# Kernel tuning notes

Measured on AMD Instinct MI355X. Metric: run time of the kernel, lower is better.

Reference implementation:

```python
import jax, jax.numpy as jnp
import numpy as np

NUM_HEADS = 16
EPS = 1e-6


def _phi(x):
    # Positive feature map: ELU + 1
    return jax.nn.elu(x) + 1.0


def setup_inputs() -> dict:
    key = jax.random.key(0)
    ks = jax.random.split(key, 5)
    B, L, D = 4, 8192, 1024
    scale = 0.02
    return {
        "x": jax.random.normal(ks[0], (B, L, D), dtype=jnp.float32),
        "Wq": jax.random.normal(ks[1], (D, D), dtype=jnp.float32) * scale,
        "Wk": jax.random.normal(ks[2], (D, D), dtype=jnp.float32) * scale,
        "Wv": jax.random.normal(ks[3], (D, D), dtype=jnp.float32) * scale,
        "Wo": jax.random.normal(ks[4], (D, D), dtype=jnp.float32) * scale,
    }


def reference(x, Wq, Wk, Wv, Wo):
    B, L, D = x.shape
    H = NUM_HEADS
    dh = D // H
    # Projections (bias-free linear layers)
    Q = x @ Wq
    K = x @ Wk
    V = x @ Wv
    # Split heads: (B, H, L, dh)
    Qh = Q.reshape(B, L, H, dh).transpose(0, 2, 1, 3)
    Kh = K.reshape(B, L, H, dh).transpose(0, 2, 1, 3)
    Vh = V.reshape(B, L, H, dh).transpose(0, 2, 1, 3)
    Qf = _phi(Qh)
    Kf = _phi(Kh)
    # Global key-value reduction over time: (B, H, dh, dh)
    Kv = jnp.einsum('bhlm,bhln->bhmn', Kf, Vh)
    # Key normalizer: (B, H, dh)
    K1 = jnp.sum(Kf, axis=2)
    # Numerator / denominator
    num = jnp.einsum('bhlm,bhmn->bhln', Qf, Kv)
    den = jnp.einsum('bhlm,bhm->bhl', Qf, K1) + EPS
    out = num / den[..., None]
    out = out.transpose(0, 2, 1, 3).reshape(B, L, D)
    return out @ Wo
```

## Files before the change

### kernel.cpp

```cpp
#include <hip/hip_runtime.h>
#include <stdint.h>
#include <stddef.h>

typedef __bf16 bf16;
typedef __attribute__((ext_vector_type(8))) __bf16 bf16x8;
typedef __attribute__((ext_vector_type(4))) __bf16 bf16x4;
typedef __attribute__((ext_vector_type(4))) float f32x4;

#define ATT_EPS 1e-6f

__device__ __forceinline__ void lds16(const void* g, void* l) {
    __builtin_amdgcn_global_load_lds(
        (const __attribute__((address_space(1))) void*)g,
        (__attribute__((address_space(3))) void*)l, 16, 0, 0);
}

__device__ __forceinline__ void swizzle_uv(int lin, int& u, int& v) {
    u = (lin & 7) | ((lin >> 6) << 3);
    v = (lin >> 3) & 7;
}

__global__ __launch_bounds__(256) void cvt_bf16(const float4* __restrict__ in,
                                                bf16x4* __restrict__ out, int n4) {
    int i = blockIdx.x * 256 + threadIdx.x;
    if (i < n4) {
        float4 v = in[i];
        bf16x4 o;
        o.x = (bf16)v.x; o.y = (bf16)v.y; o.z = (bf16)v.z; o.w = (bf16)v.w;
        out[i] = o;
    }
}

__global__ __launch_bounds__(256) void transpose_w(const float* __restrict__ W,
                                                   bf16* __restrict__ Wt) {
    __shared__ float tile[32][33];
    const int bx = blockIdx.x * 32, by = blockIdx.y * 32;
    const int tx = threadIdx.x, ty = threadIdx.y;
#pragma unroll
    for (int j = 0; j < 32; j += 8)
        tile[ty + j][tx] = W[(size_t)(by + ty + j) * 1024 + bx + tx];
    __syncthreads();
#pragma unroll
    for (int j = 0; j < 32; j += 8)
        Wt[(size_t)(bx + ty + j) * 1024 + by + tx] = (bf16)tile[tx][ty + j];
}

template <int MODE>
__global__ __launch_bounds__(256) void gemm_bt(const bf16* __restrict__ A, int lda,
                                               const bf16* __restrict__ B, int ldb,
                                               void* __restrict__ C, int ldc, int K) {
    constexpr int EP_STRIDE = 136;
    constexpr int SMEM_ELEMS = (MODE == 2) ? 128 * EP_STRIDE : 8192;
    __shared__ bf16 smem[SMEM_ELEMS] __attribute__((aligned(16)));
    bf16* sA = smem;
    bf16* sB = smem + 4096;
    const int t = threadIdx.x;
    const int wave = t >> 6;
    const int lane = t & 63;
    int u, v;
    swizzle_uv(blockIdx.x, u, v);
    const int tileM = u * 128;
    const int tileN = v * 128;
    const int wm = (wave >> 1) * 64;
    const int wn = (wave & 1) * 64;

    f32x4 acc[4][4] = {};

    const int srow = t >> 2;
    const int scol = (t & 3) * 8;
    const bf16* a0 = A + (size_t)(tileM + srow) * lda + scol;
    const bf16* a1 = A + (size_t)(tileM + 64 + srow) * lda + scol;
    const bf16* b0 = B + (size_t)(tileN + srow) * ldb + scol;
    const bf16* b1 = B + (size_t)(tileN + 64 + srow) * ldb + scol;
    bf16* dA0 = sA + wave * 512;
    bf16* dA1 = sA + 2048 + wave * 512;
    bf16* dB0 = sB + wave * 512;
    bf16* dB1 = sB + 2048 + wave * 512;

    const int rm = lane & 15;
    const int qk = (lane >> 4) * 8;

    for (int k0 = 0; k0 < K; k0 += 32) {
        lds16(a0 + k0, dA0);
        lds16(a1 + k0, dA1);
        lds16(b0 + k0, dB0);
        lds16(b1 + k0, dB1);
        __builtin_amdgcn_s_waitcnt(0);
        __syncthreads();
        bf16x8 af[4], bfr[4];
#pragma unroll
        for (int mi = 0; mi < 4; mi++)
            af[mi] = *(const bf16x8*)&sA[(wm + mi * 16 + rm) * 32 + qk];
#pragma unroll
        for (int ni = 0; ni < 4; ni++)
            bfr[ni] = *(const bf16x8*)&sB[(wn + ni * 16 + rm) * 32 + qk];
#pragma unroll
        for (int mi = 0; mi < 4; mi++)
#pragma unroll
            for (int ni = 0; ni < 4; ni++)
                acc[mi][ni] = __builtin_amdgcn_mfma_f32_16x16x32_bf16(
                    af[mi], bfr[ni], acc[mi][ni], 0, 0, 0);
        __syncthreads();
    }

    const int row0 = (lane >> 4) * 4;
    const int col = lane & 15;
    if (MODE == 0) {
#pragma unroll
        for (int mi = 0; mi < 4; mi++)
#pragma unroll
            for (int ni = 0; ni < 4; ni++)
#pragma unroll
                for (int r = 0; r < 4; r++) {
                    int gm = tileM + wm + mi * 16 + row0 + r;
                    int gn = tileN + wn + ni * 16 + col;
                    ((float*)C)[(size_t)gm * ldc + gn] = acc[mi][ni][r];
                }
    } else {
#pragma unroll
        for (int mi = 0; mi < 4; mi++)
#pragma unroll
            for (int ni = 0; ni < 4; ni++)
#pragma unroll
                for (int r = 0; r < 4; r++) {
                    float val = acc[mi][ni][r];
                    val = (val > 0.f) ? (val + 1.f) : __expf(val);
                    smem[(wm + mi * 16 + row0 + r) * EP_STRIDE + wn + ni * 16 + col] =
                        (bf16)val;
                }
        __syncthreads();
        const int er = t >> 4, ec = (t & 15) * 8;
#pragma unroll
        for (int i = 0; i < 8; i++) {
            int row = er + i * 16;
            *(bf16x8*)&((bf16*)C)[(size_t)(tileM + row) * ldc + tileN + ec] =
                *(const bf16x8*)&smem[row * EP_STRIDE + ec];
        }
    }
}

__global__ __launch_bounds__(256, 2) void kv_proj(const bf16* __restrict__ Wkt,
                                                  const bf16* __restrict__ Wvt,
                                                  const bf16* __restrict__ xb,
                                                  bf16* __restrict__ Kft,
                                                  bf16* __restrict__ Vt) {
    constexpr int EP_STRIDE = 136;
    __shared__ bf16 smem[128 * EP_STRIDE] __attribute__((aligned(16)));
    bf16* sK = smem;
    bf16* sV = smem + 4096;
    bf16* sX = smem + 8192;
    const int t = threadIdx.x;
    const int wave = t >> 6;
    const int lane = t & 63;
    int u, v;
    swizzle_uv(blockIdx.x, u, v);
    const int tileM = v * 128;
    const int tileN = u * 128;
    const int wm = (wave >> 1) * 64;
    const int wn = (wave & 1) * 64;

    f32x4 accK[4][4] = {};
    f32x4 accV[4][4] = {};

    const int srow = t >> 2;
    const int scol = (t & 3) * 8;
    const bf16* k0p = Wkt + (size_t)(tileM + srow) * 1024 + scol;
    const bf16* k1p = k0p + (size_t)64 * 1024;
    const bf16* v0p = Wvt + (size_t)(tileM + srow) * 1024 + scol;
    const bf16* v1p = v0p + (size_t)64 * 1024;
    const bf16* x0p = xb + (size_t)(tileN + srow) * 1024 + scol;
    const bf16* x1p = x0p + (size_t)64 * 1024;
    bf16* dK0 = sK + wave * 512;
    bf16* dK1 = sK + 2048 + wave * 512;
    bf16* dV0 = sV + wave * 512;
    bf16* dV1 = sV + 2048 + wave * 512;
    bf16* dX0 = sX + wave * 512;
    bf16* dX1 = sX + 2048 + wave * 512;

    const int rm = lane & 15;
    const int qk = (lane >> 4) * 8;

    for (int k0 = 0; k0 < 1024; k0 += 32) {
        lds16(k0p + k0, dK0);
        lds16(k1p + k0, dK1);
        lds16(v0p + k0, dV0);
        lds16(v1p + k0, dV1);
        lds16(x0p + k0, dX0);
        lds16(x1p + k0, dX1);
        __builtin_amdgcn_s_waitcnt(0);
        __syncthreads();
        bf16x8 bfr[4], afK[4], afV[4];
#pragma unroll
        for (int ni = 0; ni < 4; ni++)
            bfr[ni] = *(const bf16x8*)&sX[(wn + ni * 16 + rm) * 32 + qk];
#pragma unroll
        for (int mi = 0; mi < 4; mi++) {
            afK[mi] = *(const bf16x8*)&sK[(wm + mi * 16 + rm) * 32 + qk];
            afV[mi] = *(const bf16x8*)&sV[(wm + mi * 16 + rm) * 32 + qk];
        }
#pragma unroll
        for (int mi = 0; mi < 4; mi++)
#pragma unroll
            for (int ni = 0; ni < 4; ni++) {
                accK[mi][ni] = __builtin_amdgcn_mfma_f32_16x16x32_bf16(
                    afK[mi], bfr[ni], accK[mi][ni], 0, 0, 0);
                accV[mi][ni] = __builtin_amdgcn_mfma_f32_16x16x32_bf16(
                    afV[mi], bfr[ni], accV[mi][ni], 0, 0, 0);
            }
        __syncthreads();
    }

    const int row0 = (lane >> 4) * 4;
    const int col = lane & 15;
    const int er = t >> 4, ec = (t & 15) * 8;

#pragma unroll
    for (int mi = 0; mi < 4; mi++)
#pragma unroll
        for (int ni = 0; ni < 4; ni++)
#pragma unroll
            for (int r = 0; r < 4; r++) {
                float val = accK[mi][ni][r];
                val = (val > 0.f) ? (val + 1.f) : __expf(val);
                smem[(wm + mi * 16 + row0 + r) * EP_STRIDE + wn + ni * 16 + col] =
                    (bf16)val;
            }
    __syncthreads();
#pragma unroll
    for (int i = 0; i < 8; i++) {
        int row = er + i * 16;
        *(bf16x8*)&Kft[(size_t)(tileM + row) * 32768 + tileN + ec] =
            *(const bf16x8*)&smem[row * EP_STRIDE + ec];
    }
    __syncthreads();
#pragma unroll
    for (int mi = 0; mi < 4; mi++)
#pragma unroll
        for (int ni = 0; ni < 4; ni++)
#pragma unroll
            for (int r = 0; r < 4; r++)
                smem[(wm + mi * 16 + row0 + r) * EP_STRIDE + wn + ni * 16 + col] =
                    (bf16)accV[mi][ni][r];
    __syncthreads();
#pragma unroll
    for (int i = 0; i < 8; i++) {
        int row = er + i * 16;
        *(bf16x8*)&Vt[(size_t)(tileM + row) * 32768 + tileN + ec] =
            *(const bf16x8*)&smem[row * EP_STRIDE + ec];
    }
}

__global__ __launch_bounds__(256) void kv_reduce(const bf16* __restrict__ Kft,
                                                 const bf16* __restrict__ Vt,
                                                 float* __restrict__ Kv) {
    const int chunk = blockIdx.x;
    const int bh = blockIdx.y;
    const int b = bh >> 4, h = bh & 15;
    __shared__ bf16 sA[64 * 32] __attribute__((aligned(16)));
    __shared__ bf16 sB[64 * 32] __attribute__((aligned(16)));
    const int t = threadIdx.x, wave = t >> 6, lane = t & 63;
    const size_t cbase = (size_t)b * 8192 + (size_t)chunk * 1024;
    const int srow = t >> 2, scol = (t & 3) * 8;
    const bf16* a0 = Kft + (size_t)(h * 64 + srow) * 32768 + cbase + scol;
    const bf16* b0 = Vt + (size_t)(h * 64 + srow) * 32768 + cbase + scol;
    bf16* dA = sA + wave * 512;
    bf16* dB = sB + wave * 512;
    const int rm = lane & 15, qk = (lane >> 4) * 8;

    f32x4 acc[4] = {};
    f32x4 acc1 = {0.f, 0.f, 0.f, 0.f};
    bf16x8 ones;
#pragma unroll
    for (int j = 0; j < 8; j++) ones[j] = (bf16)1.0f;

    for (int k0 = 0; k0 < 1024; k0 += 32) {
        lds16(a0 + k0, dA);
        lds16(b0 + k0, dB);
        __builtin_amdgcn_s_waitcnt(0);
        __syncthreads();
        bf16x8 af = *(const bf16x8*)&sA[(wave * 16 + rm) * 32 + qk];
        bf16x8 bfr[4];
#pragma unroll
        for (int ni = 0; ni < 4; ni++)
            bfr[ni] = *(const bf16x8*)&sB[(ni * 16 + rm) * 32 + qk];
#pragma unroll
        for (int ni = 0; ni < 4; ni++)
            acc[ni] = __builtin_amdgcn_mfma_f32_16x16x32_bf16(af, bfr[ni], acc[ni], 0, 0, 0);
        acc1 = __builtin_amdgcn_mfma_f32_16x16x32_bf16(af, ones, acc1, 0, 0, 0);
        __syncthreads();
    }

    float* out = Kv + bh * 65 * 64;
    const int row0 = (lane >> 4) * 4, col = lane & 15;
    const int m0 = wave * 16 + row0;
#pragma unroll
    for (int ni = 0; ni < 4; ni++)
#pragma unroll
        for (int r = 0; r < 4; r++)
            atomicAdd(&out[(ni * 16 + col) * 64 + m0 + r], acc[ni][r]);
    if (col == 0) {
#pragma unroll
        for (int r = 0; r < 4; r++) atomicAdd(&out[64 * 64 + m0 + r], acc1[r]);
    }
}

__global__ __launch_bounds__(256) void attn_out(const bf16* __restrict__ Qf,
                                                const float* __restrict__ Kv,
                                                bf16* __restrict__ attn) {
    const int lt = blockIdx.x;
    const int bh = blockIdx.y;
    const int b = bh >> 4, h = bh & 15;
    constexpr int EP_STRIDE = 80;
    __shared__ bf16 smem[13312] __attribute__((aligned(16)));
    __shared__ float den[128];
    bf16* sQ = smem;
    bf16* sB = smem + 8192;
    const int t = threadIdx.x, wave = t >> 6, lane = t & 63;
    const int qrow = t >> 3, qc = (t & 7) * 8;
    const bf16* qp = Qf + (size_t)(b * 8192 + lt * 128 + qrow) * 1024 + h * 64 + qc;
#pragma unroll
    for (int i = 0; i < 4; i++)
        lds16(qp + (size_t)i * 32 * 1024, sQ + i * 2048 + wave * 512);
    const float* kv = Kv + bh * 65 * 64;
    for (int idx = t; idx < 80 * 64; idx += 256) {
        int n = idx >> 6, k2 = idx & 63;
        sB[idx] = (n < 65) ? (bf16)kv[n * 64 + k2] : (bf16)0.f;
    }
    __builtin_amdgcn_s_waitcnt(0);
    __syncthreads();

    f32x4 acc[2][5] = {};
    const int rm = lane & 15, qk = (lane >> 4) * 8;
#pragma unroll
    for (int k0 = 0; k0 < 64; k0 += 32) {
        bf16x8 af[2], bfr[5];
#pragma unroll
        for (int mi = 0; mi < 2; mi++)
            af[mi] = *(const bf16x8*)&sQ[(wave * 32 + mi * 16 + rm) * 64 + k0 + qk];
#pragma unroll
        for (int ni = 0; ni < 5; ni++)
            bfr[ni] = *(const bf16x8*)&sB[(ni * 16 + rm) * 64 + k0 + qk];
#pragma unroll
        for (int mi = 0; mi < 2; mi++)
#pragma unroll
            for (int ni = 0; ni < 5; ni++)
                acc[mi][ni] = __builtin_amdgcn_mfma_f32_16x16x32_bf16(
                    af[mi], bfr[ni], acc[mi][ni], 0, 0, 0);
    }

    const int row0 = (lane >> 4) * 4, col = lane & 15;
    if (col == 0) {
#pragma unroll
        for (int mi = 0; mi < 2; mi++)
#pragma unroll
            for (int r = 0; r < 4; r++)
                den[wave * 32 + mi * 16 + row0 + r] = acc[mi][4][r] + ATT_EPS;
    }
    __syncthreads();
#pragma unroll
    for (int mi = 0; mi < 2; mi++)
#pragma unroll
        for (int ni = 0; ni < 4; ni++)
#pragma unroll
            for (int r = 0; r < 4; r++) {
                int rl = wave * 32 + mi * 16 + row0 + r;
                smem[rl * EP_STRIDE + ni * 16 + col] =
                    (bf16)(acc[mi][ni][r] / den[rl]);
            }
    __syncthreads();
    const int er = t >> 3, ec = (t & 7) * 8;
#pragma unroll
    for (int i = 0; i < 4; i++) {
        int row = er + i * 32;
        *(bf16x8*)&attn[(size_t)(b * 8192 + lt * 128 + row) * 1024 + h * 64 + ec] =
            *(const bf16x8*)&smem[row * EP_STRIDE + ec];
    }
}

extern "C" void kernel_launch(void* const* d_in, const int* in_sizes, int n_in,
                              void* d_out, int out_size, void* d_ws, size_t ws_size,
                              hipStream_t stream) {
    const float* x  = (const float*)d_in[0];
    const float* Wq = (const float*)d_in[1];
    const float* Wk = (const float*)d_in[2];
    const float* Wv = (const float*)d_in[3];
    const float* Wo = (const float*)d_in[4];

    char* ws = (char*)d_ws;
    bf16* xb  = (bf16*)ws;
    bf16* Qf  = (bf16*)(ws + ((size_t)64 << 20));
    bf16* Kft = (bf16*)(ws + ((size_t)128 << 20));
    bf16* Vt  = (bf16*)(ws + ((size_t)192 << 20));
    bf16* Wqt = (bf16*)(ws + ((size_t)256 << 20));
    bf16* Wkt = Wqt + 1024 * 1024;
    bf16* Wvt = Wkt + 1024 * 1024;
    bf16* Wot = Wvt + 1024 * 1024;
    float* Kv = (float*)(Wot + 1024 * 1024);
    bf16* attn = xb;

    cvt_bf16<<<8388608 / 256, 256, 0, stream>>>((const float4*)x, (bf16x4*)xb, 8388608);
    dim3 tb(32, 8);
    transpose_w<<<dim3(32, 32), tb, 0, stream>>>(Wq, Wqt);
    transpose_w<<<dim3(32, 32), tb, 0, stream>>>(Wk, Wkt);
    transpose_w<<<dim3(32, 32), tb, 0, stream>>>(Wv, Wvt);
    transpose_w<<<dim3(32, 32), tb, 0, stream>>>(Wo, Wot);
    hipMemsetAsync(Kv, 0, (size_t)64 * 65 * 64 * sizeof(float), stream);

    gemm_bt<2><<<2048, 256, 0, stream>>>(xb, 1024, Wqt, 1024, Qf, 1024, 1024);
    kv_proj<<<2048, 256, 0, stream>>>(Wkt, Wvt, xb, Kft, Vt);
    kv_reduce<<<dim3(8, 64), 256, 0, stream>>>(Kft, Vt, Kv);
    attn_out<<<dim3(64, 64), 256, 0, stream>>>(Qf, Kv, attn);
    gemm_bt<0><<<2048, 256, 0, stream>>>(attn, 1024, Wot, 1024, d_out, 1024, 1024);
}
```

Baseline: 689.7 us.

## Replace GEMMs with 256x256 tiled, 4-stage pipelined, swizzled-LDS kernel

Replaces the 128x128 single-buffered GEMM and the fused K/V projection kernel with one 256x256-tile, 512-thread GEMM. It uses a 4-deep LDS ring buffer with async global-to-LDS loads, XOR-swizzled LDS layout, MFMA priority bumps and an XCD-aware block remap. The K and V projections become two separate launches, so x is read twice instead of once. The 128KB LDS footprint limits occupancy to one block per CU, and correctness depends on the swizzle and vmcnt counting being right.

```diff
diff --git a/kernel.cpp b/kernel.cpp
--- a/kernel.cpp
+++ b/kernel.cpp
@@ -13,11 +13,6 @@
     __builtin_amdgcn_global_load_lds(
         (const __attribute__((address_space(1))) void*)g,
         (__attribute__((address_space(3))) void*)l, 16, 0, 0);
-}
-
-__device__ __forceinline__ void swizzle_uv(int lin, int& u, int& v) {
-    u = (lin & 7) | ((lin >> 6) << 3);
-    v = (lin >> 3) & 7;
 }
 
 __global__ __launch_bounds__(256) void cvt_bf16(const float4* __restrict__ in,
@@ -46,207 +41,119 @@
 }
 
 template <int MODE>
-__global__ __launch_bounds__(256) void gemm_bt(const bf16* __restrict__ A, int lda,
+__global__ __launch_bounds__(512) void gemm256(const bf16* __restrict__ A, int lda,
                                                const bf16* __restrict__ B, int ldb,
-                                               void* __restrict__ C, int ldc, int K) {
-    constexpr int EP_STRIDE = 136;
-    constexpr int SMEM_ELEMS = (MODE == 2) ? 128 * EP_STRIDE : 8192;
-    __shared__ bf16 smem[SMEM_ELEMS] __attribute__((aligned(16)));
-    bf16* sA = smem;
-    bf16* sB = smem + 4096;
+                                               void* __restrict__ C, int ldc,
+                                               int K, int fast_m, int fl2) {
+    __shared__ bf16 smem[65536] __attribute__((aligned(16)));
     const int t = threadIdx.x;
-    const int wave = t >> 6;
-    const int lane = t & 63;
-    int u, v;
-    swizzle_uv(blockIdx.x, u, v);
-    const int tileM = u * 128;
-    const int tileN = v * 128;
-    const int wm = (wave >> 1) * 64;
-    const int wn = (wave & 1) * 64;
-
-    f32x4 acc[4][4] = {};
-
-    const int srow = t >> 2;
-    const int scol = (t & 3) * 8;
-    const bf16* a0 = A + (size_t)(tileM + srow) * lda + scol;
-    const bf16* a1 = A + (size_t)(tileM + 64 + srow) * lda + scol;
-    const bf16* b0 = B + (size_t)(tileN + srow) * ldb + scol;
-    const bf16* b1 = B + (size_t)(tileN + 64 + srow) * ldb + scol;
-    bf16* dA0 = sA + wave * 512;
-    bf16* dA1 = sA + 2048 + wave * 512;
-    bf16* dB0 = sB + wave * 512;
-    bf16* dB1 = sB + 2048 + wave * 512;
-
-    const int rm = lane & 15;
-    const int qk = (lane >> 4) * 8;
-
-    for (int k0 = 0; k0 < K; k0 += 32) {
-        lds16(a0 + k0, dA0);
-        lds16(a1 + k0, dA1);
-        lds16(b0 + k0, dB0);
-        lds16(b1 + k0, dB1);
-        __builtin_amdgcn_s_waitcnt(0);
-        __syncthreads();
-        bf16x8 af[4], bfr[4];
-#pragma unroll
-        for (int mi = 0; mi < 4; mi++)
-            af[mi] = *(const bf16x8*)&sA[(wm + mi * 16 + rm) * 32 + qk];
-#pragma unroll
-        for (int ni = 0; ni < 4; ni++)
-            bfr[ni] = *(const bf16x8*)&sB[(wn + ni * 16 + rm) * 32 + qk];
-#pragma unroll
-        for (int mi = 0; mi < 4; mi++)
+    const int wave = t >> 6, lane = t & 63;
+    const int q8 = gridDim.x >> 3;
+    const int wg = (blockIdx.x & 7) * q8 + (blockIdx.x >> 3);
+    const int f = wg & ((1 << fl2) - 1), s = wg >> fl2;
+    const int mt = fast_m ? f : s, nt = fast_m ? s : f;
+    const int tileM = mt << 8, tileN = nt << 8;
+    const int wm = wave >> 2, wn = wave & 3;
+
+    int rowS[2], colS[2];
+#pragma unroll
+    for (int j = 0; j < 2; j++) {
+        int off = t * 16 + j * 8192;
+        int o = off & 1023;
+        int op = o ^ (((o >> 9) & 1) << 5);
+        rowS[j] = (off >> 10) * 16 + (op >> 6);
+        colS[j] = (op & 63) >> 1;
+    }
+    const int rm = lane & 15, qq = lane >> 4;
+    const int foff = ((rm * 64 + qq * 16) ^ ((rm >> 3) << 5)) >> 1;
+
+    f32x4 acc[8][4] = {};
+
+#define STAGE(tt)                                                              \
+    {                                                                          \
+        bf16* sA_ = smem + ((tt) & 3) * 16384;                                 \
+        bf16* sB_ = sA_ + 8192;                                                \
+        const int k0_ = (tt) << 5;                                             \
+        _Pragma("unroll") for (int j = 0; j < 2; j++) {                        \
+            lds16(A + (size_t)(tileM + rowS[j]) * lda + k0_ + colS[j],         \
+                  sA_ + wave * 512 + j * 4096);                                \
+            lds16(B + (size_t)(tileN + rowS[j]) * ldb + k0_ + colS[j],         \
+                  sB_ + wave * 512 + j * 4096);                                \
+        }                                                                      \
+    }
+
+#define COMPUTE(tt)                                                            \
+    {                                                                          \
+        const bf16* pA_ = smem + ((tt) & 3) * 16384 + wm * 4096 + foff;        \
+        const bf16* pB_ = smem + ((tt) & 3) * 16384 + 8192 + wn * 2048 + foff; \
+        bf16x8 af_[8], bv_[4];                                                 \
+        _Pragma("unroll") for (int mi = 0; mi < 8; mi++)                       \
+            af_[mi] = *(const bf16x8*)(pA_ + mi * 512);                        \
+        _Pragma("unroll") for (int ni = 0; ni < 4; ni++)                       \
+            bv_[ni] = *(const bf16x8*)(pB_ + ni * 512);                        \
+        __builtin_amdgcn_s_setprio(1);                                         \
+        _Pragma("unroll") for (int mi = 0; mi < 8; mi++)                       \
+            _Pragma("unroll") for (int ni = 0; ni < 4; ni++)                   \
+                acc[mi][ni] = __builtin_amdgcn_mfma_f32_16x16x32_bf16(         \
+                    af_[mi], bv_[ni], acc[mi][ni], 0, 0, 0);                   \
+        __builtin_amdgcn_s_setprio(0);                                         \
+    }
+
+#define SYNCV(n)                                                               \
+    asm volatile("s_waitcnt vmcnt(" #n ")" ::: "memory");                      \
+    __builtin_amdgcn_s_barrier();                                              \
+    __builtin_amdgcn_sched_barrier(0);
+
+    const int NT = K >> 5;
+    STAGE(0); STAGE(1); STAGE(2);
+    SYNCV(8);
+    for (int tt = 0; tt < NT - 3; ++tt) {
+        STAGE(tt + 3);
+        COMPUTE(tt);
+        SYNCV(8);
+    }
+    COMPUTE(NT - 3); SYNCV(4);
+    COMPUTE(NT - 2); SYNCV(0);
+    COMPUTE(NT - 1);
+#undef STAGE
+#undef COMPUTE
+#undef SYNCV
+
+    const int row0 = (lane >> 4) * 4, col = lane & 15;
+    if (MODE == 0) {
+        float* Cf = (float*)C;
+#pragma unroll
+        for (int mi = 0; mi < 8; mi++)
 #pragma unroll
             for (int ni = 0; ni < 4; ni++)
-                acc[mi][ni] = __builtin_amdgcn_mfma_f32_16x16x32_bf16(
-                    af[mi], bfr[ni], acc[mi][ni], 0, 0, 0);
-        __syncthreads();
-    }
-
-    const int row0 = (lane >> 4) * 4;
-    const int col = lane & 15;
-    if (MODE == 0) {
-#pragma unroll
-        for (int mi = 0; mi < 4; mi++)
-#pragma unroll
-            for (int ni = 0; ni < 4; ni++)
 #pragma unroll
                 for (int r = 0; r < 4; r++) {
-                    int gm = tileM + wm + mi * 16 + row0 + r;
-                    int gn = tileN + wn + ni * 16 + col;
-                    ((float*)C)[(size_t)gm * ldc + gn] = acc[mi][ni][r];
+                    int gm = tileM + wm * 128 + mi * 16 + row0 + r;
+                    int gn = tileN + wn * 64 + ni * 16 + col;
+                    Cf[(size_t)gm * ldc + gn] = acc[mi][ni][r];
                 }
     } else {
-#pragma unroll
-        for (int mi = 0; mi < 4; mi++)
+        __syncthreads();
+        bf16* Cb = (bf16*)C;
+#pragma unroll
+        for (int mi = 0; mi < 8; mi++)
 #pragma unroll
             for (int ni = 0; ni < 4; ni++)
 #pragma unroll
                 for (int r = 0; r < 4; r++) {
-                    float val = acc[mi][ni][r];
-                    val = (val > 0.f) ? (val + 1.f) : __expf(val);
-                    smem[(wm + mi * 16 + row0 + r) * EP_STRIDE + wn + ni * 16 + col] =
-                        (bf16)val;
+                    float v = acc[mi][ni][r];
+                    if (MODE == 2) v = (v > 0.f) ? (v + 1.f) : __expf(v);
+                    smem[(wm * 128 + mi * 16 + row0 + r) * 256 +
+                         wn * 64 + ni * 16 + col] = (bf16)v;
                 }
         __syncthreads();
-        const int er = t >> 4, ec = (t & 15) * 8;
-#pragma unroll
-        for (int i = 0; i < 8; i++) {
-            int row = er + i * 16;
-            *(bf16x8*)&((bf16*)C)[(size_t)(tileM + row) * ldc + tileN + ec] =
-                *(const bf16x8*)&smem[row * EP_STRIDE + ec];
+#pragma unroll
+        for (int i = 0; i < 16; i++) {
+            int c = t + i * 512;
+            int row = c >> 5, cb = (c & 31) * 8;
+            *(bf16x8*)&Cb[(size_t)(tileM + row) * ldc + tileN + cb] =
+                *(const bf16x8*)&smem[row * 256 + cb];
         }
-    }
-}
-
-__global__ __launch_bounds__(256, 2) void kv_proj(const bf16* __restrict__ Wkt,
-                                                  const bf16* __restrict__ Wvt,
-                                                  const bf16* __restrict__ xb,
-                                                  bf16* __restrict__ Kft,
-                                                  bf16* __restrict__ Vt) {
-    constexpr int EP_STRIDE = 136;
-    __shared__ bf16 smem[128 * EP_STRIDE] __attribute__((aligned(16)));
-    bf16* sK = smem;
-    bf16* sV = smem + 4096;
-    bf16* sX = smem + 8192;
-    const int t = threadIdx.x;
-    const int wave = t >> 6;
-    const int lane = t & 63;
-    int u, v;
-    swizzle_uv(blockIdx.x, u, v);
-    const int tileM = v * 128;
-    const int tileN = u * 128;
-    const int wm = (wave >> 1) * 64;
-    const int wn = (wave & 1) * 64;
-
-    f32x4 accK[4][4] = {};
-    f32x4 accV[4][4] = {};
-
-    const int srow = t >> 2;
-    const int scol = (t & 3) * 8;
-    const bf16* k0p = Wkt + (size_t)(tileM + srow) * 1024 + scol;
-    const bf16* k1p = k0p + (size_t)64 * 1024;
-    const bf16* v0p = Wvt + (size_t)(tileM + srow) * 1024 + scol;
-    const bf16* v1p = v0p + (size_t)64 * 1024;
-    const bf16* x0p = xb + (size_t)(tileN + srow) * 1024 + scol;
-    const bf16* x1p = x0p + (size_t)64 * 1024;
-    bf16* dK0 = sK + wave * 512;
-    bf16* dK1 = sK + 2048 + wave * 512;
-    bf16* dV0 = sV + wave * 512;
-    bf16* dV1 = sV + 2048 + wave * 512;
-    bf16* dX0 = sX + wave * 512;
-    bf16* dX1 = sX + 2048 + wave * 512;
-
-    const int rm = lane & 15;
-    const int qk = (lane >> 4) * 8;
-
-    for (int k0 = 0; k0 < 1024; k0 += 32) {
-        lds16(k0p + k0, dK0);
-        lds16(k1p + k0, dK1);
-        lds16(v0p + k0, dV0);
-        lds16(v1p + k0, dV1);
-        lds16(x0p + k0, dX0);
-        lds16(x1p + k0, dX1);
-        __builtin_amdgcn_s_waitcnt(0);
-        __syncthreads();
-        bf16x8 bfr[4], afK[4], afV[4];
-#pragma unroll
-        for (int ni = 0; ni < 4; ni++)
-            bfr[ni] = *(const bf16x8*)&sX[(wn + ni * 16 + rm) * 32 + qk];
-#pragma unroll
-        for (int mi = 0; mi < 4; mi++) {
-            afK[mi] = *(const bf16x8*)&sK[(wm + mi * 16 + rm) * 32 + qk];
-            afV[mi] = *(const bf16x8*)&sV[(wm + mi * 16 + rm) * 32 + qk];
-        }
-#pragma unroll
-        for (int mi = 0; mi < 4; mi++)
-#pragma unroll
-            for (int ni = 0; ni < 4; ni++) {
-                accK[mi][ni] = __builtin_amdgcn_mfma_f32_16x16x32_bf16(
-                    afK[mi], bfr[ni], accK[mi][ni], 0, 0, 0);
-                accV[mi][ni] = __builtin_amdgcn_mfma_f32_16x16x32_bf16(
-                    afV[mi], bfr[ni], accV[mi][ni], 0, 0, 0);
-            }
-        __syncthreads();
-    }
-
-    const int row0 = (lane >> 4) * 4;
-    const int col = lane & 15;
-    const int er = t >> 4, ec = (t & 15) * 8;
-
-#pragma unroll
-    for (int mi = 0; mi < 4; mi++)
-#pragma unroll
-        for (int ni = 0; ni < 4; ni++)
-#pragma unroll
-            for (int r = 0; r < 4; r++) {
-                float val = accK[mi][ni][r];
-                val = (val > 0.f) ? (val + 1.f) : __expf(val);
-                smem[(wm + mi * 16 + row0 + r) * EP_STRIDE + wn + ni * 16 + col] =
-                    (bf16)val;
-            }
-    __syncthreads();
-#pragma unroll
-    for (int i = 0; i < 8; i++) {
-        int row = er + i * 16;
-        *(bf16x8*)&Kft[(size_t)(tileM + row) * 32768 + tileN + ec] =
-            *(const bf16x8*)&smem[row * EP_STRIDE + ec];
-    }
-    __syncthreads();
-#pragma unroll
-    for (int mi = 0; mi < 4; mi++)
-#pragma unroll
-        for (int ni = 0; ni < 4; ni++)
-#pragma unroll
-            for (int r = 0; r < 4; r++)
-                smem[(wm + mi * 16 + row0 + r) * EP_STRIDE + wn + ni * 16 + col] =
-                    (bf16)accV[mi][ni][r];
-    __syncthreads();
-#pragma unroll
-    for (int i = 0; i < 8; i++) {
-        int row = er + i * 16;
-        *(bf16x8*)&Vt[(size_t)(tileM + row) * 32768 + tileN + ec] =
-            *(const bf16x8*)&smem[row * EP_STRIDE + ec];
     }
 }
 
@@ -406,9 +313,10 @@
     transpose_w<<<dim3(32, 32), tb, 0, stream>>>(Wo, Wot);
     hipMemsetAsync(Kv, 0, (size_t)64 * 65 * 64 * sizeof(float), stream);
 
-    gemm_bt<2><<<2048, 256, 0, stream>>>(xb, 1024, Wqt, 1024, Qf, 1024, 1024);
-    kv_proj<<<2048, 256, 0, stream>>>(Wkt, Wvt, xb, Kft, Vt);
+    gemm256<2><<<512, 512, 0, stream>>>(xb, 1024, Wqt, 1024, Qf, 1024, 1024, 0, 2);
+    gemm256<2><<<512, 512, 0, stream>>>(Wkt, 1024, xb, 1024, Kft, 32768, 1024, 1, 2);
+    gemm256<1><<<512, 512, 0, stream>>>(Wvt, 1024, xb, 1024, Vt, 32768, 1024, 1, 2);
     kv_reduce<<<dim3(8, 64), 256, 0, stream>>>(Kft, Vt, Kv);
     attn_out<<<dim3(64, 64), 256, 0, stream>>>(Qf, Kv, attn);
-    gemm_bt<0><<<2048, 256, 0, stream>>>(attn, 1024, Wot, 1024, d_out, 1024, 1024);
-}
+    gemm256<0><<<512, 512, 0, stream>>>(attn, 1024, Wot, 1024, d_out, 1024, 1024, 0, 2);
+}
```

Result: faster. 635.2 us (-7.9%).
